# Kernel tuning notes

Hardware: AMD Instinct MI355X
Metric: run time of the kernel (lower is better)

## Reference

```python
import jax, jax.numpy as jnp
import numpy as np

DIM = 1024
NUM_EXPERTS = 8
HIDDEN = 4096
CAP_FACTOR = 2.0
B, S = 4, 2048


def setup_inputs() -> dict:
    key = jax.random.key(0)
    ks = jax.random.split(key, 6)
    scale_r = 1.0 / np.sqrt(DIM)
    scale_1 = 1.0 / np.sqrt(DIM)
    scale_2 = 1.0 / np.sqrt(HIDDEN)
    return {
        "x": jax.random.normal(ks[0], (B, S, DIM), dtype=jnp.float32),
        # router: nn.Linear(dim, num_experts, bias=False) -> weight [E, D]
        "router_w": jax.random.uniform(ks[1], (NUM_EXPERTS, DIM), jnp.float32, -scale_r, scale_r),
        # stacked expert MLP params
        "w1": jax.random.uniform(ks[2], (NUM_EXPERTS, DIM, HIDDEN), jnp.float32, -scale_1, scale_1),
        "b1": jax.random.uniform(ks[3], (NUM_EXPERTS, HIDDEN), jnp.float32, -scale_1, scale_1),
        "w2": jax.random.uniform(ks[4], (NUM_EXPERTS, HIDDEN, DIM), jnp.float32, -scale_2, scale_2),
        "b2": jax.random.uniform(ks[5], (NUM_EXPERTS, DIM), jnp.float32, -scale_2, scale_2),
    }


def reference(x, router_w, w1, b1, w2, b2):
    # x: [B, S, D]
    Bz, Sz, Dz = x.shape
    E = router_w.shape[0]
    capacity = max(1, int(Sz * CAP_FACTOR / E) + 1)

    # router softmax over experts: [B, S, E]
    scores = jax.nn.softmax(jnp.einsum("bsd,ed->bse", x, router_w), axis=-1)

    # expert-choice: each expert picks top-C tokens. [B, E, S] -> [B, E, C]
    scores_t = jnp.swapaxes(scores, 1, 2)
    gate_vals, sel_idx = jax.lax.top_k(scores_t, capacity)

    # gather selected tokens: [B, E, C, D]
    b_idx = jnp.arange(Bz)[:, None, None]
    tokens = x[b_idx, sel_idx]

    # batched expert MLP (GELU exact, matching nn.GELU default)
    h = jnp.einsum("becd,edh->bech", tokens, w1) + b1[None, :, None, :]
    h = jax.nn.gelu(h, approximate=False)
    y = jnp.einsum("bech,ehd->becd", h, w2) + b2[None, :, None, :]

    # gate and scatter-add combine back to [B, S, D]
    gated = y * gate_vals[..., None]
    out = jnp.zeros_like(x).at[b_idx, sel_idx].add(gated)
    return out
```

## Files before the change

kernel.cpp:

```cpp
#include <hip/hip_runtime.h>
#include <cstdint>

#define DIMD  1024
#define NEXP  8
#define HIDN  4096
#define BATCH 4
#define SEQ   2048
#define CAPC  513
#define RPEX  2176
#define TPEX  17
#define MTOT  (NEXP * RPEX)
#define MTILES (MTOT / 128)

typedef __bf16 bf16x8 __attribute__((ext_vector_type(8)));
typedef float  f32x4  __attribute__((ext_vector_type(4)));

__device__ __forceinline__ unsigned short f2bf(float f) {
    unsigned u = __float_as_uint(f);
    unsigned r = (u + 0x7FFFu + ((u >> 16) & 1u)) >> 16;
    return (unsigned short)r;
}

__device__ __forceinline__ void gl16(const unsigned short* g, unsigned short* l) {
    __builtin_amdgcn_global_load_lds(
        (const __attribute__((address_space(1))) void*)g,
        (__attribute__((address_space(3))) void*)l, 16, 0, 0);
}

__device__ __forceinline__ void swz_grp(int GY, int& bx, int& by) {
    int xcd = blockIdx.x & 7, pos = blockIdx.x >> 3;
    int tps = TPEX * GY;
    int sc = pos / tps, rem = pos - sc * tps;
    int bxl = rem / GY, byIn = rem - bxl * GY;
    bx = xcd * TPEX + bxl;
    by = sc * GY + byIn;
}

__global__ __launch_bounds__(64)
void router_kernel(const float* __restrict__ x, const float* __restrict__ rw,
                   float* __restrict__ scores) {
    int token = blockIdx.x;
    int lane  = threadIdx.x;
    const float4* xr = reinterpret_cast<const float4*>(x + (size_t)token * DIMD);
    float4 xv[4];
#pragma unroll
    for (int j = 0; j < 4; ++j) xv[j] = xr[lane * 4 + j];
    float acc[NEXP];
#pragma unroll
    for (int e = 0; e < NEXP; ++e) {
        const float4* wr = reinterpret_cast<const float4*>(rw + (size_t)e * DIMD);
        float a = 0.f;
#pragma unroll
        for (int j = 0; j < 4; ++j) {
            float4 wv = wr[lane * 4 + j];
            a += xv[j].x * wv.x; a += xv[j].y * wv.y;
            a += xv[j].z * wv.z; a += xv[j].w * wv.w;
        }
#pragma unroll
        for (int off = 32; off > 0; off >>= 1) a += __shfl_xor(a, off);
        acc[e] = a;
    }
    float m = acc[0];
#pragma unroll
    for (int e = 1; e < NEXP; ++e) m = fmaxf(m, acc[e]);
    float s = 0.f;
#pragma unroll
    for (int e = 0; e < NEXP; ++e) { acc[e] = expf(acc[e] - m); s += acc[e]; }
    float inv = 1.f / s;
    if (lane == 0) {
        int b = token >> 11;
        int t = token & (SEQ - 1);
#pragma unroll
        for (int e = 0; e < NEXP; ++e)
            scores[((size_t)(b * NEXP + e)) * SEQ + t] = acc[e] * inv;
    }
}

__global__ __launch_bounds__(256)
void topk_kernel(const float* __restrict__ scores, int* __restrict__ sel,
                 float* __restrict__ gate, int* __restrict__ cnt,
                 int* __restrict__ invmap) {
    int be    = blockIdx.x >> 3;
    int chunk = blockIdx.x & 7;
    const float* sc = scores + (size_t)be * SEQ;
    __shared__ float s_sc[SEQ];
    int t = threadIdx.x;
#pragma unroll
    for (int q = 0; q < 8; ++q) s_sc[t + q * 256] = sc[t + q * 256];
    __syncthreads();
    int i = chunk * 256 + t;
    float v = s_sc[i];
    int r = 0;
#pragma unroll 8
    for (int j = 0; j < SEQ; ++j) {
        float u = s_sc[j];
        r += (u > v) || (u == v && j < i);
    }
    if (r < CAPC) {
        sel [(size_t)be * CAPC + r] = i;
        gate[(size_t)be * CAPC + r] = v;
        int b = be >> 3, e = be & 7;
        int tok = b * SEQ + i;
        int p = atomicAdd(cnt + tok, 1);
        invmap[(size_t)tok * 8 + p] = e * RPEX + b * CAPC + r;
    }
}

__global__ __launch_bounds__(256)
void gather_kernel(const float* __restrict__ x, const int* __restrict__ sel,
                   unsigned short* __restrict__ dhi) {
    int gr = blockIdx.x;
    int e  = gr / RPEX;
    int rl = gr - e * RPEX;
    int t  = threadIdx.x;
    size_t dbase = (size_t)gr * DIMD + t * 4;
    if (rl < BATCH * CAPC) {
        int b = rl / CAPC, c = rl - b * CAPC;
        int tok = sel[(size_t)(b * NEXP + e) * CAPC + c];
        float4 v = *reinterpret_cast<const float4*>(x + ((size_t)(b * SEQ + tok)) * DIMD + t * 4);
        ushort4 h;
        h.x = f2bf(v.x); h.y = f2bf(v.y); h.z = f2bf(v.z); h.w = f2bf(v.w);
        *reinterpret_cast<ushort4*>(dhi + dbase) = h;
    } else {
        ushort4 z = {0, 0, 0, 0};
        *reinterpret_cast<ushort4*>(dhi + dbase) = z;
    }
}

__global__ __launch_bounds__(256)
void convT_kernel(const float* __restrict__ src, unsigned short* __restrict__ dhi,
                  int Nsrc, size_t srcEStride, int k0, int n0, int kLen, int nLen) {
    int e = blockIdx.z;
    src += (size_t)e * srcEStride;
    dhi += (size_t)e * kLen * nLen;
    int kb = blockIdx.x * 64, nb = blockIdx.y * 64;
    __shared__ float T[64][65];
    int t = threadIdx.x;
    for (int i = t; i < 1024; i += 256) {
        int r = i >> 4, c4 = (i & 15) * 4;
        float4 v = *reinterpret_cast<const float4*>(
            src + (size_t)(k0 + kb + r) * Nsrc + n0 + nb + c4);
        T[r][c4 + 0] = v.x; T[r][c4 + 1] = v.y; T[r][c4 + 2] = v.z; T[r][c4 + 3] = v.w;
    }
    __syncthreads();
    for (int i = t; i < 1024; i += 256) {
        int n = i >> 4, kc = (i & 15) * 4;
        ushort4 h;
        h.x = f2bf(T[kc + 0][n]); h.y = f2bf(T[kc + 1][n]);
        h.z = f2bf(T[kc + 2][n]); h.w = f2bf(T[kc + 3][n]);
        *reinterpret_cast<ushort4*>(dhi + (size_t)(nb + n) * kLen + kb + kc) = h;
    }
}


#define GEMM_PRE(Abase, Bbase, Kc)                                              \
    int t = threadIdx.x;                                                        \
    int l = t & 63, wid = t >> 6;                                               \
    int wr = wid >> 1, wc = wid & 1;                                            \
    int grp = l >> 4, li = l & 15;                                              \
    int fsw  = (grp ^ ((li >> 1) & 3)) * 8;                                     \
    int gsrc = ((l & 3) ^ ((l >> 3) & 3)) * 8;                                  \
    int ra0 = (wid * 2) * 16 + (l >> 2);                                        \
    int ra1 = ra0 + 16;                                                         \
    __shared__ __align__(16) unsigned short As[3][4096];                        \
    __shared__ __align__(16) unsigned short Bs[3][4096];                        \
    int regA = wid * 1024;                                                      \
    const unsigned short* gA0 = (Abase) + (size_t)(bx * 128 + ra0) * (Kc) + gsrc; \
    const unsigned short* gA1 = (Abase) + (size_t)(bx * 128 + ra1) * (Kc) + gsrc; \
    const unsigned short* gB0 = (Bbase) + (size_t)(bn + ra0) * (Kc) + gsrc;     \
    const unsigned short* gB1 = (Bbase) + (size_t)(bn + ra1) * (Kc) + gsrc;     \
    f32x4 acc[4][4];                                                            \
    _Pragma("unroll")                                                           \
    for (int m = 0; m < 4; ++m)                                                 \
        _Pragma("unroll")                                                       \
        for (int n = 0; n < 4; ++n) { f32x4 z = {0.f,0.f,0.f,0.f}; acc[m][n] = z; }

#define STAGE(buf, kt) do {                                                     \
    gl16(gA0 + (kt), &As[buf][regA]);                                           \
    gl16(gA1 + (kt), &As[buf][regA + 512]);                                     \
    gl16(gB0 + (kt), &Bs[buf][regA]);                                           \
    gl16(gB1 + (kt), &Bs[buf][regA + 512]); } while (0)

#define GEMM_LOOP(Kc) do {                                                      \
    const int NT = (Kc) / 32;                                                   \
    STAGE(0, 0);                                                                \
    STAGE(1, 32);                                                               \
    int cb = 0;                                                                 \
    for (int tt = 0; tt < NT; ++tt) {                                           \
        if (tt == NT - 1) asm volatile("s_waitcnt vmcnt(0)" ::: "memory");      \
        else              asm volatile("s_waitcnt vmcnt(4)" ::: "memory");      \
        __builtin_amdgcn_s_barrier();                                           \
        int sb = cb + 2; if (sb >= 3) sb -= 3;                                  \
        if (tt + 2 < NT) STAGE(sb, (tt + 2) * 32);                              \
        bf16x8 ah[4], bh[4];                                                    \
        const unsigned short* aB = &As[cb][wr * 2048 + li * 32 + fsw];          \
        const unsigned short* bB = &Bs[cb][wc * 2048 + li * 32 + fsw];          \
        ah[0] = *(const bf16x8*)(aB);        ah[1] = *(const bf16x8*)(aB + 512); \
        ah[2] = *(const bf16x8*)(aB + 1024); ah[3] = *(const bf16x8*)(aB + 1536); \
        bh[0] = *(const bf16x8*)(bB);        bh[1] = *(const bf16x8*)(bB + 512); \
        bh[2] = *(const bf16x8*)(bB + 1024); bh[3] = *(const bf16x8*)(bB + 1536); \
        __builtin_amdgcn_s_setprio(1);                                          \
        _Pragma("unroll")                                                       \
        for (int m = 0; m < 4; ++m)                                             \
            _Pragma("unroll")                                                   \
            for (int n = 0; n < 4; ++n)                                         \
                acc[m][n] = __builtin_amdgcn_mfma_f32_16x16x32_bf16(            \
                    ah[m], bh[n], acc[m][n], 0, 0, 0);                          \
        __builtin_amdgcn_s_setprio(0);                                          \
        ++cb; if (cb == 3) cb = 0;                                              \
    } } while (0)

__global__ __launch_bounds__(256)
void gemm1_mfma(const unsigned short* __restrict__ Ahi,
                const unsigned short* __restrict__ Whi,
                const float* __restrict__ bias, unsigned short* __restrict__ Hhi,
                size_t wstride, int nbias0, int ldh, int GY) {
    const int K = DIMD;
    int bx, by; swz_grp(GY, bx, by);
    int bn = by * 128;
    int e = bx / TPEX;
    const unsigned short* Bh = Whi + (size_t)e * wstride;

    GEMM_PRE(Ahi, Bh, K)
    GEMM_LOOP(K);

    int hr0 = bx * 128 + wr * 64;
    int cb2 = bn + wc * 64;
    const float cc0 = 0.044715f;
    const float cc1 = -2.302118131f;
#pragma unroll
    for (int m = 0; m < 4; ++m)
#pragma unroll
        for (int q = 0; q < 4; ++q) {
            int row = hr0 + m * 16 + grp * 4 + q;
#pragma unroll
            for (int n = 0; n < 4; ++n) {
                int col = cb2 + n * 16 + li;
                float v = acc[m][n][q] + bias[(size_t)e * HIDN + nbias0 + col];
                float p = __builtin_fmaf(cc0 * v, v * v, v);
                float g = v * __builtin_amdgcn_rcpf(1.0f + exp2f(cc1 * p));
                Hhi[(size_t)row * ldh + col] = f2bf(g);
            }
        }
}

__global__ __launch_bounds__(256)
void gemm2_mfma(const unsigned short* __restrict__ Ahi,
                const unsigned short* __restrict__ Whi,
                const float* __restrict__ bias, const float* __restrict__ gate,
                float* __restrict__ Y, size_t wstride, int K, int GY) {
    int bx, by; swz_grp(GY, bx, by);
    int bn = by * 128;
    int e = bx / TPEX;
    int rbase_e = (bx - e * TPEX) * 128;
    const unsigned short* Bh = Whi + (size_t)e * wstride;

    GEMM_PRE(Ahi, Bh, K)
    GEMM_LOOP(K);

    int cb2 = bn + wc * 64;
#pragma unroll
    for (int m = 0; m < 4; ++m)
#pragma unroll
        for (int q = 0; q < 4; ++q) {
            int off = wr * 64 + m * 16 + grp * 4 + q;
            int rloc = rbase_e + off;
            if (rloc < BATCH * CAPC) {
                int b = rloc / CAPC, c = rloc - b * CAPC;
                float g = gate[(size_t)(b * NEXP + e) * CAPC + c];
                size_t grow = (size_t)bx * 128 + off;
#pragma unroll
                for (int n = 0; n < 4; ++n) {
                    int col = cb2 + n * 16 + li;
                    float v = acc[m][n][q];
                    size_t yo = grow * DIMD + col;
                    if (bias) Y[yo] = g * (v + bias[(size_t)e * DIMD + col]);
                    else      Y[yo] = Y[yo] + g * v;
                }
            }
        }
}

__global__ __launch_bounds__(64)
void combine_kernel(const float* __restrict__ Y, const int* __restrict__ cnt,
                    const int* __restrict__ invmap, float* __restrict__ out) {
    int tok = blockIdx.x;
    int lane = threadIdx.x;
    int n = cnt[tok];
    f32x4 acc[4];
#pragma unroll
    for (int q = 0; q < 4; ++q) { f32x4 z = {0.f, 0.f, 0.f, 0.f}; acc[q] = z; }
#pragma unroll
    for (int j = 0; j < 8; ++j) {
        if (j < n) {
            int row = invmap[(size_t)tok * 8 + j];
            const f32x4* yr = reinterpret_cast<const f32x4*>(Y + (size_t)row * DIMD);
#pragma unroll
            for (int q = 0; q < 4; ++q) acc[q] += yr[q * 64 + lane];
        }
    }
    f32x4* op = reinterpret_cast<f32x4*>(out + (size_t)tok * DIMD);
#pragma unroll
    for (int q = 0; q < 4; ++q) op[q * 64 + lane] = acc[q];
}

extern "C" void kernel_launch(void* const* d_in, const int* in_sizes, int n_in,
                              void* d_out, int out_size, void* d_ws, size_t ws_size,
                              hipStream_t stream) {
    (void)in_sizes; (void)n_in; (void)out_size;
    const float* x  = (const float*)d_in[0];
    const float* rw = (const float*)d_in[1];
    const float* w1 = (const float*)d_in[2];
    const float* b1 = (const float*)d_in[3];
    const float* w2 = (const float*)d_in[4];
    const float* b2 = (const float*)d_in[5];
    float* out = (float*)d_out;

    char* ws = (char*)d_ws;
    size_t off = 0;
    auto alloc = [&](size_t bytes) -> char* {
        char* p = ws + off;
        off = (off + bytes + 255) & ~(size_t)255;
        return p;
    };

    float* scores = (float*)alloc((size_t)BATCH * NEXP * SEQ * 4);
    int*   sel    = (int*)  alloc((size_t)BATCH * NEXP * CAPC * 4);
    float* gate   = (float*)alloc((size_t)BATCH * NEXP * CAPC * 4);
    int*   cnt    = (int*)  alloc((size_t)BATCH * SEQ * 4);
    int*   invmap = (int*)  alloc((size_t)BATCH * SEQ * 8 * 4);
    float* Y      = (float*)alloc((size_t)MTOT * DIMD * 4);
    size_t common = off;

    const size_t A1B = (size_t)MTOT * DIMD * 2;
    int C = 8;
    for (int c = 1; c <= 8; c <<= 1) {
        size_t wc = (size_t)NEXP * (HIDN / c) * DIMD * 2;
        size_t hc = (size_t)MTOT * (HIDN / c) * 2;
        size_t need = common + A1B + 2 * wc + hc + (8u << 20);
        if (need <= ws_size) { C = c; break; }
    }
    const int HN = HIDN / C;
    const int nY1 = HN / 128;
    const int GY1 = (nY1 < 8) ? nY1 : 8;

    unsigned short* A1h = (unsigned short*)alloc(A1B);
    size_t WCB = (size_t)NEXP * HN * DIMD * 2;
    size_t HCB = (size_t)MTOT * HN * 2;
    unsigned short* W1h = (unsigned short*)alloc(WCB);
    unsigned short* W2h = (unsigned short*)alloc(WCB);
    unsigned short* Hh  = (unsigned short*)alloc(HCB);

    hipMemsetAsync(cnt, 0, (size_t)BATCH * SEQ * 4, stream);
    router_kernel<<<BATCH * SEQ, 64, 0, stream>>>(x, rw, scores);
    topk_kernel<<<BATCH * NEXP * 8, 256, 0, stream>>>(scores, sel, gate, cnt, invmap);
    gather_kernel<<<MTOT, 256, 0, stream>>>(x, sel, A1h);

    for (int c = 0; c < C; ++c) {
        convT_kernel<<<dim3(DIMD / 64, HN / 64, NEXP), 256, 0, stream>>>(
            w1, W1h, HIDN, (size_t)DIMD * HIDN, 0, c * HN, DIMD, HN);
        gemm1_mfma<<<MTILES * nY1, 256, 0, stream>>>(
            A1h, W1h, b1, Hh, (size_t)HN * DIMD, c * HN, HN, GY1);
        convT_kernel<<<dim3(HN / 64, DIMD / 64, NEXP), 256, 0, stream>>>(
            w2, W2h, DIMD, (size_t)HIDN * DIMD, c * HN, 0, HN, DIMD);
        gemm2_mfma<<<MTILES * (DIMD / 128), 256, 0, stream>>>(
            Hh, W2h, (c == 0) ? b2 : nullptr, gate, Y,
            (size_t)DIMD * HN, HN, 4);
    }
    combine_kernel<<<BATCH * SEQ, 64, 0, stream>>>(Y, cnt, invmap, out);
}
```

Before: 619.6 us.

## Widen GEMM tiles to 128x256 and split-K gemm2 into two partial outputs

Both expert GEMMs now use 128x256 output tiles, with each wave computing a 4x8 grid of MFMA fragments and a larger B buffer in shared memory, so each A tile is reused across more columns. gemm2 splits K in two, writing partial sums to separate Y0/Y1 buffers that the combine kernel adds together, which keeps the grid large despite the wider tiles. gemm1 loads its bias values into registers once before the epilogue. The cost is higher register and LDS use per block, which may lower occupancy, plus an extra fp32 Y buffer and more combine traffic.

```diff
diff --git a/kernel.cpp b/kernel.cpp
--- a/kernel.cpp
+++ b/kernel.cpp
@@ -25,15 +25,6 @@
     __builtin_amdgcn_global_load_lds(
         (const __attribute__((address_space(1))) void*)g,
         (__attribute__((address_space(3))) void*)l, 16, 0, 0);
-}
-
-__device__ __forceinline__ void swz_grp(int GY, int& bx, int& by) {
-    int xcd = blockIdx.x & 7, pos = blockIdx.x >> 3;
-    int tps = TPEX * GY;
-    int sc = pos / tps, rem = pos - sc * tps;
-    int bxl = rem / GY, byIn = rem - bxl * GY;
-    bx = xcd * TPEX + bxl;
-    by = sc * GY + byIn;
 }
 
 __global__ __launch_bounds__(64)
@@ -153,79 +144,88 @@
 }
 
 
-#define GEMM_PRE(Abase, Bbase, Kc)                                              \
+#define GEMM_PRE(Abase, LDA, Bbase, LDB)                                        \
     int t = threadIdx.x;                                                        \
     int l = t & 63, wid = t >> 6;                                               \
     int wr = wid >> 1, wc = wid & 1;                                            \
     int grp = l >> 4, li = l & 15;                                              \
     int fsw  = (grp ^ ((li >> 1) & 3)) * 8;                                     \
     int gsrc = ((l & 3) ^ ((l >> 3) & 3)) * 8;                                  \
-    int ra0 = (wid * 2) * 16 + (l >> 2);                                        \
-    int ra1 = ra0 + 16;                                                         \
-    __shared__ __align__(16) unsigned short As[3][4096];                        \
-    __shared__ __align__(16) unsigned short Bs[3][4096];                        \
-    int regA = wid * 1024;                                                      \
-    const unsigned short* gA0 = (Abase) + (size_t)(bx * 128 + ra0) * (Kc) + gsrc; \
-    const unsigned short* gA1 = (Abase) + (size_t)(bx * 128 + ra1) * (Kc) + gsrc; \
-    const unsigned short* gB0 = (Bbase) + (size_t)(bn + ra0) * (Kc) + gsrc;     \
-    const unsigned short* gB1 = (Bbase) + (size_t)(bn + ra1) * (Kc) + gsrc;     \
-    f32x4 acc[4][4];                                                            \
+    __shared__ __align__(16) unsigned short As[3][4096];         \
+    __shared__ __align__(16) unsigned short Bs[3][8192];         \
+    int dst = wid * 512;                                                        \
+    const unsigned short* gA0 = (Abase) + (size_t)(bx * 128 + wid * 16 + (l >> 2)) * (LDA) + gsrc; \
+    const unsigned short* gA1 = gA0 + (size_t)64 * (LDA);                       \
+    const unsigned short* gB0 = (Bbase) + (size_t)(bn + wid * 16 + (l >> 2)) * (LDB) + gsrc; \
+    const unsigned short* gB1 = gB0 + (size_t)64  * (LDB);                      \
+    const unsigned short* gB2 = gB0 + (size_t)128 * (LDB);                      \
+    const unsigned short* gB3 = gB0 + (size_t)192 * (LDB);                      \
+    f32x4 acc[4][8];                                                            \
     _Pragma("unroll")                                                           \
     for (int m = 0; m < 4; ++m)                                                 \
         _Pragma("unroll")                                                       \
-        for (int n = 0; n < 4; ++n) { f32x4 z = {0.f,0.f,0.f,0.f}; acc[m][n] = z; }
+        for (int n = 0; n < 8; ++n) { f32x4 z = {0.f,0.f,0.f,0.f}; acc[m][n] = z; }
 
 #define STAGE(buf, kt) do {                                                     \
-    gl16(gA0 + (kt), &As[buf][regA]);                                           \
-    gl16(gA1 + (kt), &As[buf][regA + 512]);                                     \
-    gl16(gB0 + (kt), &Bs[buf][regA]);                                           \
-    gl16(gB1 + (kt), &Bs[buf][regA + 512]); } while (0)
-
-#define GEMM_LOOP(Kc) do {                                                      \
-    const int NT = (Kc) / 32;                                                   \
+    gl16(gA0 + (kt), &As[buf][dst]);                                            \
+    gl16(gA1 + (kt), &As[buf][2048 + dst]);                                     \
+    gl16(gB0 + (kt), &Bs[buf][dst]);                                            \
+    gl16(gB1 + (kt), &Bs[buf][2048 + dst]);                                     \
+    gl16(gB2 + (kt), &Bs[buf][4096 + dst]);                                     \
+    gl16(gB3 + (kt), &Bs[buf][6144 + dst]); } while (0)
+
+#define GEMM_LOOP(NT) do {                                                      \
     STAGE(0, 0);                                                                \
     STAGE(1, 32);                                                               \
     int cb = 0;                                                                 \
-    for (int tt = 0; tt < NT; ++tt) {                                           \
-        if (tt == NT - 1) asm volatile("s_waitcnt vmcnt(0)" ::: "memory");      \
-        else              asm volatile("s_waitcnt vmcnt(4)" ::: "memory");      \
+    for (int tt = 0; tt < (NT); ++tt) {                                         \
+        if (tt == (NT) - 1) asm volatile("s_waitcnt vmcnt(0)" ::: "memory");    \
+        else                asm volatile("s_waitcnt vmcnt(6)" ::: "memory");    \
         __builtin_amdgcn_s_barrier();                                           \
         int sb = cb + 2; if (sb >= 3) sb -= 3;                                  \
-        if (tt + 2 < NT) STAGE(sb, (tt + 2) * 32);                              \
-        bf16x8 ah[4], bh[4];                                                    \
+        if (tt + 2 < (NT)) STAGE(sb, (tt + 2) * 32);                            \
+        bf16x8 af[4], bfv[8];                                                   \
         const unsigned short* aB = &As[cb][wr * 2048 + li * 32 + fsw];          \
-        const unsigned short* bB = &Bs[cb][wc * 2048 + li * 32 + fsw];          \
-        ah[0] = *(const bf16x8*)(aB);        ah[1] = *(const bf16x8*)(aB + 512); \
-        ah[2] = *(const bf16x8*)(aB + 1024); ah[3] = *(const bf16x8*)(aB + 1536); \
-        bh[0] = *(const bf16x8*)(bB);        bh[1] = *(const bf16x8*)(bB + 512); \
-        bh[2] = *(const bf16x8*)(bB + 1024); bh[3] = *(const bf16x8*)(bB + 1536); \
+        const unsigned short* bB = &Bs[cb][wc * 4096 + li * 32 + fsw];          \
+        _Pragma("unroll")                                                       \
+        for (int m = 0; m < 4; ++m) af[m]  = *(const bf16x8*)(aB + m * 512);    \
+        _Pragma("unroll")                                                       \
+        for (int n = 0; n < 8; ++n) bfv[n] = *(const bf16x8*)(bB + n * 512);    \
         __builtin_amdgcn_s_setprio(1);                                          \
         _Pragma("unroll")                                                       \
         for (int m = 0; m < 4; ++m)                                             \
             _Pragma("unroll")                                                   \
-            for (int n = 0; n < 4; ++n)                                         \
+            for (int n = 0; n < 8; ++n)                                         \
                 acc[m][n] = __builtin_amdgcn_mfma_f32_16x16x32_bf16(            \
-                    ah[m], bh[n], acc[m][n], 0, 0, 0);                          \
+                    af[m], bfv[n], acc[m][n], 0, 0, 0);                         \
         __builtin_amdgcn_s_setprio(0);                                          \
         ++cb; if (cb == 3) cb = 0;                                              \
     } } while (0)
 
 __global__ __launch_bounds__(256)
-void gemm1_mfma(const unsigned short* __restrict__ Ahi,
-                const unsigned short* __restrict__ Whi,
+void gemm1_mfma(const unsigned short* __restrict__ A,
+                const unsigned short* __restrict__ W,
                 const float* __restrict__ bias, unsigned short* __restrict__ Hhi,
                 size_t wstride, int nbias0, int ldh, int GY) {
     const int K = DIMD;
-    int bx, by; swz_grp(GY, bx, by);
-    int bn = by * 128;
+    int xcd = blockIdx.x & 7, pos = blockIdx.x >> 3;
+    int tps = TPEX * GY;
+    int sc = pos / tps, rem = pos - sc * tps;
+    int bxl = rem / GY, byIn = rem - bxl * GY;
+    int bx = xcd * TPEX + bxl;
+    int bn = (sc * GY + byIn) * 256;
     int e = bx / TPEX;
-    const unsigned short* Bh = Whi + (size_t)e * wstride;
-
-    GEMM_PRE(Ahi, Bh, K)
-    GEMM_LOOP(K);
+    const unsigned short* Bb = W + (size_t)e * wstride;
+
+    GEMM_PRE(A, K, Bb, K)
+    GEMM_LOOP(K / 32);
 
     int hr0 = bx * 128 + wr * 64;
-    int cb2 = bn + wc * 64;
+    int cb2 = bn + wc * 128;
+    float bv[8];
+#pragma unroll
+    for (int n = 0; n < 8; ++n)
+        bv[n] = bias[(size_t)e * HIDN + nbias0 + cb2 + n * 16 + li];
     const float cc0 = 0.044715f;
     const float cc1 = -2.302118131f;
 #pragma unroll
@@ -234,9 +234,9 @@
         for (int q = 0; q < 4; ++q) {
             int row = hr0 + m * 16 + grp * 4 + q;
 #pragma unroll
-            for (int n = 0; n < 4; ++n) {
+            for (int n = 0; n < 8; ++n) {
                 int col = cb2 + n * 16 + li;
-                float v = acc[m][n][q] + bias[(size_t)e * HIDN + nbias0 + col];
+                float v = acc[m][n][q] + bv[n];
                 float p = __builtin_fmaf(cc0 * v, v * v, v);
                 float g = v * __builtin_amdgcn_rcpf(1.0f + exp2f(cc1 * p));
                 Hhi[(size_t)row * ldh + col] = f2bf(g);
@@ -245,20 +245,28 @@
 }
 
 __global__ __launch_bounds__(256)
-void gemm2_mfma(const unsigned short* __restrict__ Ahi,
-                const unsigned short* __restrict__ Whi,
-                const float* __restrict__ bias, const float* __restrict__ gate,
-                float* __restrict__ Y, size_t wstride, int K, int GY) {
-    int bx, by; swz_grp(GY, bx, by);
-    int bn = by * 128;
+void gemm2_mfma(const unsigned short* __restrict__ Hh,
+                const unsigned short* __restrict__ W2,
+                const float* __restrict__ bias, int init,
+                const float* __restrict__ gate,
+                float* __restrict__ Y0, float* __restrict__ Y1,
+                size_t wstride, int lda, int Kb) {
+    int xcd = blockIdx.x & 7, pos = blockIdx.x >> 3;
+    int ks = pos / (TPEX * 4);
+    int rem = pos - ks * (TPEX * 4);
+    int bxl = rem >> 2, by = rem & 3;
+    int bx = xcd * TPEX + bxl;
+    int bn = by * 256;
     int e = bx / TPEX;
     int rbase_e = (bx - e * TPEX) * 128;
-    const unsigned short* Bh = Whi + (size_t)e * wstride;
-
-    GEMM_PRE(Ahi, Bh, K)
-    GEMM_LOOP(K);
-
-    int cb2 = bn + wc * 64;
+    const unsigned short* Ab = Hh + (size_t)ks * Kb;
+    const unsigned short* Bb = W2 + (size_t)e * wstride + (size_t)ks * Kb;
+
+    GEMM_PRE(Ab, lda, Bb, lda)
+    GEMM_LOOP(Kb / 32);
+
+    float* Yp = ks ? Y1 : Y0;
+    int cb2 = bn + wc * 128;
 #pragma unroll
     for (int m = 0; m < 4; ++m)
 #pragma unroll
@@ -270,20 +278,22 @@
                 float g = gate[(size_t)(b * NEXP + e) * CAPC + c];
                 size_t grow = (size_t)bx * 128 + off;
 #pragma unroll
-                for (int n = 0; n < 4; ++n) {
+                for (int n = 0; n < 8; ++n) {
                     int col = cb2 + n * 16 + li;
                     float v = acc[m][n][q];
+                    if (ks == 0 && bias) v += bias[(size_t)e * DIMD + col];
                     size_t yo = grow * DIMD + col;
-                    if (bias) Y[yo] = g * (v + bias[(size_t)e * DIMD + col]);
-                    else      Y[yo] = Y[yo] + g * v;
+                    if (init) Yp[yo] = g * v;
+                    else      Yp[yo] = Yp[yo] + g * v;
                 }
             }
         }
 }
 
 __global__ __launch_bounds__(64)
-void combine_kernel(const float* __restrict__ Y, const int* __restrict__ cnt,
-                    const int* __restrict__ invmap, float* __restrict__ out) {
+void combine_kernel(const float* __restrict__ Y0, const float* __restrict__ Y1,
+                    const int* __restrict__ cnt, const int* __restrict__ invmap,
+                    float* __restrict__ out) {
     int tok = blockIdx.x;
     int lane = threadIdx.x;
     int n = cnt[tok];
@@ -294,9 +304,10 @@
     for (int j = 0; j < 8; ++j) {
         if (j < n) {
             int row = invmap[(size_t)tok * 8 + j];
-            const f32x4* yr = reinterpret_cast<const f32x4*>(Y + (size_t)row * DIMD);
-#pragma unroll
-            for (int q = 0; q < 4; ++q) acc[q] += yr[q * 64 + lane];
+            const f32x4* y0 = reinterpret_cast<const f32x4*>(Y0 + (size_t)row * DIMD);
+            const f32x4* y1 = reinterpret_cast<const f32x4*>(Y1 + (size_t)row * DIMD);
+#pragma unroll
+            for (int q = 0; q < 4; ++q) acc[q] += y0[q * 64 + lane] + y1[q * 64 + lane];
         }
     }
     f32x4* op = reinterpret_cast<f32x4*>(out + (size_t)tok * DIMD);
@@ -329,7 +340,8 @@
     float* gate   = (float*)alloc((size_t)BATCH * NEXP * CAPC * 4);
     int*   cnt    = (int*)  alloc((size_t)BATCH * SEQ * 4);
     int*   invmap = (int*)  alloc((size_t)BATCH * SEQ * 8 * 4);
-    float* Y      = (float*)alloc((size_t)MTOT * DIMD * 4);
+    float* Y0     = (float*)alloc((size_t)MTOT * DIMD * 4);
+    float* Y1     = (float*)alloc((size_t)MTOT * DIMD * 4);
     size_t common = off;
 
     const size_t A1B = (size_t)MTOT * DIMD * 2;
@@ -341,8 +353,8 @@
         if (need <= ws_size) { C = c; break; }
     }
     const int HN = HIDN / C;
-    const int nY1 = HN / 128;
-    const int GY1 = (nY1 < 8) ? nY1 : 8;
+    const int nY1 = HN / 256;
+    const int GY1 = (nY1 < 4) ? nY1 : 4;
 
     unsigned short* A1h = (unsigned short*)alloc(A1B);
     size_t WCB = (size_t)NEXP * HN * DIMD * 2;
@@ -363,9 +375,9 @@
             A1h, W1h, b1, Hh, (size_t)HN * DIMD, c * HN, HN, GY1);
         convT_kernel<<<dim3(HN / 64, DIMD / 64, NEXP), 256, 0, stream>>>(
             w2, W2h, DIMD, (size_t)HIDN * DIMD, c * HN, 0, HN, DIMD);
-        gemm2_mfma<<<MTILES * (DIMD / 128), 256, 0, stream>>>(
-            Hh, W2h, (c == 0) ? b2 : nullptr, gate, Y,
-            (size_t)DIMD * HN, HN, 4);
-    }
-    combine_kernel<<<BATCH * SEQ, 64, 0, stream>>>(Y, cnt, invmap, out);
-}
+        gemm2_mfma<<<MTILES * 4 * 2, 256, 0, stream>>>(
+            Hh, W2h, (c == 0) ? b2 : nullptr, (c == 0) ? 1 : 0, gate, Y0, Y1,
+            (size_t)DIMD * HN, HN, HN / 2);
+    }
+    combine_kernel<<<BATCH * SEQ, 64, 0, stream>>>(Y0, Y1, cnt, invmap, out);
+}
```

Result: slower. 957.1 us (+54.5%).

## Split-K the second expert GEMM into two partial outputs summed in combine

Applied to the files above, without the earlier changes.

The down-projection GEMM now splits its K dimension in two, launching twice as many workgroups. Each half writes to its own fp32 buffer (Y0/Y1), and the combine kernel sums both. Block indexing is remapped so each XCD gets a contiguous set of M tiles, improving L2 locality. The goal is to fill the GPU better when the grid of 136x8 tiles underutilizes the CUs, at the cost of an extra 70MB fp32 buffer write/read and doubled combine reads.

```diff
diff --git a/kernel.cpp b/kernel.cpp
--- a/kernel.cpp
+++ b/kernel.cpp
@@ -153,7 +153,7 @@
 }
 
 
-#define GEMM_PRE(Abase, Bbase, Kc)                                              \
+#define GEMM_PRE(Abase, LDA, Bbase, LDB)                                        \
     int t = threadIdx.x;                                                        \
     int l = t & 63, wid = t >> 6;                                               \
     int wr = wid >> 1, wc = wid & 1;                                            \
@@ -165,10 +165,10 @@
     __shared__ __align__(16) unsigned short As[3][4096];                        \
     __shared__ __align__(16) unsigned short Bs[3][4096];                        \
     int regA = wid * 1024;                                                      \
-    const unsigned short* gA0 = (Abase) + (size_t)(bx * 128 + ra0) * (Kc) + gsrc; \
-    const unsigned short* gA1 = (Abase) + (size_t)(bx * 128 + ra1) * (Kc) + gsrc; \
-    const unsigned short* gB0 = (Bbase) + (size_t)(bn + ra0) * (Kc) + gsrc;     \
-    const unsigned short* gB1 = (Bbase) + (size_t)(bn + ra1) * (Kc) + gsrc;     \
+    const unsigned short* gA0 = (Abase) + (size_t)(bx * 128 + ra0) * (LDA) + gsrc; \
+    const unsigned short* gA1 = (Abase) + (size_t)(bx * 128 + ra1) * (LDA) + gsrc; \
+    const unsigned short* gB0 = (Bbase) + (size_t)(bn + ra0) * (LDB) + gsrc;    \
+    const unsigned short* gB1 = (Bbase) + (size_t)(bn + ra1) * (LDB) + gsrc;    \
     f32x4 acc[4][4];                                                            \
     _Pragma("unroll")                                                           \
     for (int m = 0; m < 4; ++m)                                                 \
@@ -181,17 +181,16 @@
     gl16(gB0 + (kt), &Bs[buf][regA]);                                           \
     gl16(gB1 + (kt), &Bs[buf][regA + 512]); } while (0)
 
-#define GEMM_LOOP(Kc) do {                                                      \
-    const int NT = (Kc) / 32;                                                   \
+#define GEMM_LOOP(NT) do {                                                      \
     STAGE(0, 0);                                                                \
     STAGE(1, 32);                                                               \
     int cb = 0;                                                                 \
-    for (int tt = 0; tt < NT; ++tt) {                                           \
-        if (tt == NT - 1) asm volatile("s_waitcnt vmcnt(0)" ::: "memory");      \
-        else              asm volatile("s_waitcnt vmcnt(4)" ::: "memory");      \
+    for (int tt = 0; tt < (NT); ++tt) {                                         \
+        if (tt == (NT) - 1) asm volatile("s_waitcnt vmcnt(0)" ::: "memory");    \
+        else                asm volatile("s_waitcnt vmcnt(4)" ::: "memory");    \
         __builtin_amdgcn_s_barrier();                                           \
         int sb = cb + 2; if (sb >= 3) sb -= 3;                                  \
-        if (tt + 2 < NT) STAGE(sb, (tt + 2) * 32);                              \
+        if (tt + 2 < (NT)) STAGE(sb, (tt + 2) * 32);                            \
         bf16x8 ah[4], bh[4];                                                    \
         const unsigned short* aB = &As[cb][wr * 2048 + li * 32 + fsw];          \
         const unsigned short* bB = &Bs[cb][wc * 2048 + li * 32 + fsw];          \
@@ -221,8 +220,8 @@
     int e = bx / TPEX;
     const unsigned short* Bh = Whi + (size_t)e * wstride;
 
-    GEMM_PRE(Ahi, Bh, K)
-    GEMM_LOOP(K);
+    GEMM_PRE(Ahi, K, Bh, K)
+    GEMM_LOOP(K / 32);
 
     int hr0 = bx * 128 + wr * 64;
     int cb2 = bn + wc * 64;
@@ -245,19 +244,27 @@
 }
 
 __global__ __launch_bounds__(256)
-void gemm2_mfma(const unsigned short* __restrict__ Ahi,
-                const unsigned short* __restrict__ Whi,
-                const float* __restrict__ bias, const float* __restrict__ gate,
-                float* __restrict__ Y, size_t wstride, int K, int GY) {
-    int bx, by; swz_grp(GY, bx, by);
+void gemm2_mfma(const unsigned short* __restrict__ Hh,
+                const unsigned short* __restrict__ W2,
+                const float* __restrict__ bias, int init,
+                const float* __restrict__ gate,
+                float* __restrict__ Y0, float* __restrict__ Y1,
+                size_t wstride, int lda, int Kb) {
+    int xcd = blockIdx.x & 7, pos = blockIdx.x >> 3;
+    int ks = pos / (TPEX * 8);
+    int rem = pos - ks * (TPEX * 8);
+    int bxl = rem >> 3, by = rem & 7;
+    int bx = xcd * TPEX + bxl;
     int bn = by * 128;
     int e = bx / TPEX;
     int rbase_e = (bx - e * TPEX) * 128;
-    const unsigned short* Bh = Whi + (size_t)e * wstride;
-
-    GEMM_PRE(Ahi, Bh, K)
-    GEMM_LOOP(K);
-
+    const unsigned short* Ab = Hh + (size_t)ks * Kb;
+    const unsigned short* Bb = W2 + (size_t)e * wstride + (size_t)ks * Kb;
+
+    GEMM_PRE(Ab, lda, Bb, lda)
+    GEMM_LOOP(Kb / 32);
+
+    float* Yp = ks ? Y1 : Y0;
     int cb2 = bn + wc * 64;
 #pragma unroll
     for (int m = 0; m < 4; ++m)
@@ -273,17 +280,19 @@
                 for (int n = 0; n < 4; ++n) {
                     int col = cb2 + n * 16 + li;
                     float v = acc[m][n][q];
+                    if (ks == 0 && bias) v += bias[(size_t)e * DIMD + col];
                     size_t yo = grow * DIMD + col;
-                    if (bias) Y[yo] = g * (v + bias[(size_t)e * DIMD + col]);
-                    else      Y[yo] = Y[yo] + g * v;
+                    if (init) Yp[yo] = g * v;
+                    else      Yp[yo] = Yp[yo] + g * v;
                 }
             }
         }
 }
 
 __global__ __launch_bounds__(64)
-void combine_kernel(const float* __restrict__ Y, const int* __restrict__ cnt,
-                    const int* __restrict__ invmap, float* __restrict__ out) {
+void combine_kernel(const float* __restrict__ Y0, const float* __restrict__ Y1,
+                    const int* __restrict__ cnt, const int* __restrict__ invmap,
+                    float* __restrict__ out) {
     int tok = blockIdx.x;
     int lane = threadIdx.x;
     int n = cnt[tok];
@@ -294,9 +303,10 @@
     for (int j = 0; j < 8; ++j) {
         if (j < n) {
             int row = invmap[(size_t)tok * 8 + j];
-            const f32x4* yr = reinterpret_cast<const f32x4*>(Y + (size_t)row * DIMD);
-#pragma unroll
-            for (int q = 0; q < 4; ++q) acc[q] += yr[q * 64 + lane];
+            const f32x4* y0 = reinterpret_cast<const f32x4*>(Y0 + (size_t)row * DIMD);
+            const f32x4* y1 = reinterpret_cast<const f32x4*>(Y1 + (size_t)row * DIMD);
+#pragma unroll
+            for (int q = 0; q < 4; ++q) acc[q] += y0[q * 64 + lane] + y1[q * 64 + lane];
         }
     }
     f32x4* op = reinterpret_cast<f32x4*>(out + (size_t)tok * DIMD);
@@ -329,7 +339,8 @@
     float* gate   = (float*)alloc((size_t)BATCH * NEXP * CAPC * 4);
     int*   cnt    = (int*)  alloc((size_t)BATCH * SEQ * 4);
     int*   invmap = (int*)  alloc((size_t)BATCH * SEQ * 8 * 4);
-    float* Y      = (float*)alloc((size_t)MTOT * DIMD * 4);
+    float* Y0     = (float*)alloc((size_t)MTOT * DIMD * 4);
+    float* Y1     = (float*)alloc((size_t)MTOT * DIMD * 4);
     size_t common = off;
 
     const size_t A1B = (size_t)MTOT * DIMD * 2;
@@ -363,9 +374,9 @@
             A1h, W1h, b1, Hh, (size_t)HN * DIMD, c * HN, HN, GY1);
         convT_kernel<<<dim3(HN / 64, DIMD / 64, NEXP), 256, 0, stream>>>(
             w2, W2h, DIMD, (size_t)HIDN * DIMD, c * HN, 0, HN, DIMD);
-        gemm2_mfma<<<MTILES * (DIMD / 128), 256, 0, stream>>>(
-            Hh, W2h, (c == 0) ? b2 : nullptr, gate, Y,
-            (size_t)DIMD * HN, HN, 4);
-    }
-    combine_kernel<<<BATCH * SEQ, 64, 0, stream>>>(Y, cnt, invmap, out);
-}
+        gemm2_mfma<<<MTILES * 8 * 2, 256, 0, stream>>>(
+            Hh, W2h, (c == 0) ? b2 : nullptr, (c == 0) ? 1 : 0, gate, Y0, Y1,
+            (size_t)DIMD * HN, HN, HN / 2);
+    }
+    combine_kernel<<<BATCH * SEQ, 64, 0, stream>>>(Y0, Y1, cnt, invmap, out);
+}
```

Result: no change. 620.5 us, median of 2 (+0.2%).

## Fold weight transpose-convert blocks into topk and GEMM launches for overlap

Applied to the files above, without the earlier changes.

Removes the standalone convT launches and instead appends extra blocks to the topk, gemm1 and gemm2 grids that transpose and convert the next weight chunk. The W1 conversion overlaps with topk, W2 with gemm1, and the next W1 chunk with gemm2. This saves launch gaps and lets memory-bound conversion run alongside compute. It relies on the chunked workspace being double-buffered correctly, and the extra blocks share the GEMM shared-memory footprint.

```diff
diff --git a/kernel.cpp b/kernel.cpp
--- a/kernel.cpp
+++ b/kernel.cpp
@@ -76,14 +76,48 @@
     }
 }
 
+__device__ __forceinline__ void convT_body(const float* __restrict__ src,
+        unsigned short* __restrict__ dhi, int Nsrc, size_t srcEStride,
+        int k0, int n0, int kLen, int nLen, int cid, float (*T)[65]) {
+    int nx = kLen >> 6, ny = nLen >> 6;
+    int e = cid / (nx * ny);
+    int r2 = cid - e * nx * ny;
+    int kb = (r2 % nx) * 64, nb = (r2 / nx) * 64;
+    src += (size_t)e * srcEStride;
+    dhi += (size_t)e * (size_t)kLen * nLen;
+    int t = threadIdx.x;
+    for (int i = t; i < 1024; i += 256) {
+        int r = i >> 4, c4 = (i & 15) * 4;
+        float4 v = *reinterpret_cast<const float4*>(
+            src + (size_t)(k0 + kb + r) * Nsrc + n0 + nb + c4);
+        T[r][c4 + 0] = v.x; T[r][c4 + 1] = v.y; T[r][c4 + 2] = v.z; T[r][c4 + 3] = v.w;
+    }
+    __syncthreads();
+    for (int i = t; i < 1024; i += 256) {
+        int n = i >> 4, kc = (i & 15) * 4;
+        ushort4 h;
+        h.x = f2bf(T[kc + 0][n]); h.y = f2bf(T[kc + 1][n]);
+        h.z = f2bf(T[kc + 2][n]); h.w = f2bf(T[kc + 3][n]);
+        *reinterpret_cast<ushort4*>(dhi + (size_t)(nb + n) * kLen + kb + kc) = h;
+    }
+}
+
 __global__ __launch_bounds__(256)
-void topk_kernel(const float* __restrict__ scores, int* __restrict__ sel,
-                 float* __restrict__ gate, int* __restrict__ cnt,
-                 int* __restrict__ invmap) {
+void topk_conv1(const float* __restrict__ scores, int* __restrict__ sel,
+                float* __restrict__ gate, int* __restrict__ cnt,
+                int* __restrict__ invmap,
+                const float* __restrict__ csrc, unsigned short* __restrict__ cdst,
+                int cNsrc, size_t cEStride, int ck0, int cn0, int ckLen, int cnLen) {
+    __shared__ __align__(16) float T[64][65];
+    if ((int)blockIdx.x >= 256) {
+        convT_body(csrc, cdst, cNsrc, cEStride, ck0, cn0, ckLen, cnLen,
+                   blockIdx.x - 256, T);
+        return;
+    }
+    float* s_sc = &T[0][0];
     int be    = blockIdx.x >> 3;
     int chunk = blockIdx.x & 7;
     const float* sc = scores + (size_t)be * SEQ;
-    __shared__ float s_sc[SEQ];
     int t = threadIdx.x;
 #pragma unroll
     for (int q = 0; q < 8; ++q) s_sc[t + q * 256] = sc[t + q * 256];
@@ -127,33 +161,8 @@
     }
 }
 
-__global__ __launch_bounds__(256)
-void convT_kernel(const float* __restrict__ src, unsigned short* __restrict__ dhi,
-                  int Nsrc, size_t srcEStride, int k0, int n0, int kLen, int nLen) {
-    int e = blockIdx.z;
-    src += (size_t)e * srcEStride;
-    dhi += (size_t)e * kLen * nLen;
-    int kb = blockIdx.x * 64, nb = blockIdx.y * 64;
-    __shared__ float T[64][65];
-    int t = threadIdx.x;
-    for (int i = t; i < 1024; i += 256) {
-        int r = i >> 4, c4 = (i & 15) * 4;
-        float4 v = *reinterpret_cast<const float4*>(
-            src + (size_t)(k0 + kb + r) * Nsrc + n0 + nb + c4);
-        T[r][c4 + 0] = v.x; T[r][c4 + 1] = v.y; T[r][c4 + 2] = v.z; T[r][c4 + 3] = v.w;
-    }
-    __syncthreads();
-    for (int i = t; i < 1024; i += 256) {
-        int n = i >> 4, kc = (i & 15) * 4;
-        ushort4 h;
-        h.x = f2bf(T[kc + 0][n]); h.y = f2bf(T[kc + 1][n]);
-        h.z = f2bf(T[kc + 2][n]); h.w = f2bf(T[kc + 3][n]);
-        *reinterpret_cast<ushort4*>(dhi + (size_t)(nb + n) * kLen + kb + kc) = h;
-    }
-}
-
-
-#define GEMM_PRE(Abase, Bbase, Kc)                                              \
+
+#define GEMM_PRE(Abase, LDA, Bbase, LDB)                                        \
     int t = threadIdx.x;                                                        \
     int l = t & 63, wid = t >> 6;                                               \
     int wr = wid >> 1, wc = wid & 1;                                            \
@@ -162,13 +171,11 @@
     int gsrc = ((l & 3) ^ ((l >> 3) & 3)) * 8;                                  \
     int ra0 = (wid * 2) * 16 + (l >> 2);                                        \
     int ra1 = ra0 + 16;                                                         \
-    __shared__ __align__(16) unsigned short As[3][4096];                        \
-    __shared__ __align__(16) unsigned short Bs[3][4096];                        \
     int regA = wid * 1024;                                                      \
-    const unsigned short* gA0 = (Abase) + (size_t)(bx * 128 + ra0) * (Kc) + gsrc; \
-    const unsigned short* gA1 = (Abase) + (size_t)(bx * 128 + ra1) * (Kc) + gsrc; \
-    const unsigned short* gB0 = (Bbase) + (size_t)(bn + ra0) * (Kc) + gsrc;     \
-    const unsigned short* gB1 = (Bbase) + (size_t)(bn + ra1) * (Kc) + gsrc;     \
+    const unsigned short* gA0 = (Abase) + (size_t)(bx * 128 + ra0) * (LDA) + gsrc; \
+    const unsigned short* gA1 = (Abase) + (size_t)(bx * 128 + ra1) * (LDA) + gsrc; \
+    const unsigned short* gB0 = (Bbase) + (size_t)(bn + ra0) * (LDB) + gsrc;    \
+    const unsigned short* gB1 = (Bbase) + (size_t)(bn + ra1) * (LDB) + gsrc;    \
     f32x4 acc[4][4];                                                            \
     _Pragma("unroll")                                                           \
     for (int m = 0; m < 4; ++m)                                                 \
@@ -181,17 +188,16 @@
     gl16(gB0 + (kt), &Bs[buf][regA]);                                           \
     gl16(gB1 + (kt), &Bs[buf][regA + 512]); } while (0)
 
-#define GEMM_LOOP(Kc) do {                                                      \
-    const int NT = (Kc) / 32;                                                   \
+#define GEMM_LOOP(NT) do {                                                      \
     STAGE(0, 0);                                                                \
     STAGE(1, 32);                                                               \
     int cb = 0;                                                                 \
-    for (int tt = 0; tt < NT; ++tt) {                                           \
-        if (tt == NT - 1) asm volatile("s_waitcnt vmcnt(0)" ::: "memory");      \
-        else              asm volatile("s_waitcnt vmcnt(4)" ::: "memory");      \
+    for (int tt = 0; tt < (NT); ++tt) {                                         \
+        if (tt == (NT) - 1) asm volatile("s_waitcnt vmcnt(0)" ::: "memory");    \
+        else                asm volatile("s_waitcnt vmcnt(4)" ::: "memory");    \
         __builtin_amdgcn_s_barrier();                                           \
         int sb = cb + 2; if (sb >= 3) sb -= 3;                                  \
-        if (tt + 2 < NT) STAGE(sb, (tt + 2) * 32);                              \
+        if (tt + 2 < (NT)) STAGE(sb, (tt + 2) * 32);                            \
         bf16x8 ah[4], bh[4];                                                    \
         const unsigned short* aB = &As[cb][wr * 2048 + li * 32 + fsw];          \
         const unsigned short* bB = &Bs[cb][wc * 2048 + li * 32 + fsw];          \
@@ -214,15 +220,24 @@
 void gemm1_mfma(const unsigned short* __restrict__ Ahi,
                 const unsigned short* __restrict__ Whi,
                 const float* __restrict__ bias, unsigned short* __restrict__ Hhi,
-                size_t wstride, int nbias0, int ldh, int GY) {
+                size_t wstride, int nbias0, int ldh, int GY, int nGemm,
+                const float* __restrict__ csrc, unsigned short* __restrict__ cdst,
+                int cNsrc, size_t cEStride, int ck0, int cn0, int ckLen, int cnLen) {
+    __shared__ __align__(16) unsigned short As[3][4096];
+    __shared__ __align__(16) unsigned short Bs[3][4096];
+    if ((int)blockIdx.x >= nGemm) {
+        convT_body(csrc, cdst, cNsrc, cEStride, ck0, cn0, ckLen, cnLen,
+                   blockIdx.x - nGemm, reinterpret_cast<float(*)[65]>(&As[0][0]));
+        return;
+    }
     const int K = DIMD;
     int bx, by; swz_grp(GY, bx, by);
     int bn = by * 128;
     int e = bx / TPEX;
     const unsigned short* Bh = Whi + (size_t)e * wstride;
 
-    GEMM_PRE(Ahi, Bh, K)
-    GEMM_LOOP(K);
+    GEMM_PRE(Ahi, K, Bh, K)
+    GEMM_LOOP(K / 32);
 
     int hr0 = bx * 128 + wr * 64;
     int cb2 = bn + wc * 64;
@@ -245,18 +260,27 @@
 }
 
 __global__ __launch_bounds__(256)
-void gemm2_mfma(const unsigned short* __restrict__ Ahi,
-                const unsigned short* __restrict__ Whi,
+void gemm2_mfma(const unsigned short* __restrict__ Hh,
+                const unsigned short* __restrict__ W2,
                 const float* __restrict__ bias, const float* __restrict__ gate,
-                float* __restrict__ Y, size_t wstride, int K, int GY) {
+                float* __restrict__ Y, size_t wstride, int K, int GY, int nGemm,
+                const float* __restrict__ csrc, unsigned short* __restrict__ cdst,
+                int cNsrc, size_t cEStride, int ck0, int cn0, int ckLen, int cnLen) {
+    __shared__ __align__(16) unsigned short As[3][4096];
+    __shared__ __align__(16) unsigned short Bs[3][4096];
+    if ((int)blockIdx.x >= nGemm) {
+        convT_body(csrc, cdst, cNsrc, cEStride, ck0, cn0, ckLen, cnLen,
+                   blockIdx.x - nGemm, reinterpret_cast<float(*)[65]>(&As[0][0]));
+        return;
+    }
     int bx, by; swz_grp(GY, bx, by);
     int bn = by * 128;
     int e = bx / TPEX;
     int rbase_e = (bx - e * TPEX) * 128;
-    const unsigned short* Bh = Whi + (size_t)e * wstride;
-
-    GEMM_PRE(Ahi, Bh, K)
-    GEMM_LOOP(K);
+    const unsigned short* Bb = W2 + (size_t)e * wstride;
+
+    GEMM_PRE(Hh, K, Bb, K)
+    GEMM_LOOP(K / 32);
 
     int cb2 = bn + wc * 64;
 #pragma unroll
@@ -351,21 +375,27 @@
     unsigned short* W2h = (unsigned short*)alloc(WCB);
     unsigned short* Hh  = (unsigned short*)alloc(HCB);
 
+    const int nCv1 = (DIMD / 64) * (HN / 64) * NEXP;
+    const int nCv2 = (HN / 64) * (DIMD / 64) * NEXP;
+
     hipMemsetAsync(cnt, 0, (size_t)BATCH * SEQ * 4, stream);
     router_kernel<<<BATCH * SEQ, 64, 0, stream>>>(x, rw, scores);
-    topk_kernel<<<BATCH * NEXP * 8, 256, 0, stream>>>(scores, sel, gate, cnt, invmap);
+    topk_conv1<<<256 + nCv1, 256, 0, stream>>>(
+        scores, sel, gate, cnt, invmap,
+        w1, W1h, HIDN, (size_t)DIMD * HIDN, 0, 0, DIMD, HN);
     gather_kernel<<<MTOT, 256, 0, stream>>>(x, sel, A1h);
 
     for (int c = 0; c < C; ++c) {
-        convT_kernel<<<dim3(DIMD / 64, HN / 64, NEXP), 256, 0, stream>>>(
-            w1, W1h, HIDN, (size_t)DIMD * HIDN, 0, c * HN, DIMD, HN);
-        gemm1_mfma<<<MTILES * nY1, 256, 0, stream>>>(
-            A1h, W1h, b1, Hh, (size_t)HN * DIMD, c * HN, HN, GY1);
-        convT_kernel<<<dim3(HN / 64, DIMD / 64, NEXP), 256, 0, stream>>>(
+        int G1 = MTILES * nY1;
+        gemm1_mfma<<<G1 + nCv2, 256, 0, stream>>>(
+            A1h, W1h, b1, Hh, (size_t)HN * DIMD, c * HN, HN, GY1, G1,
             w2, W2h, DIMD, (size_t)HIDN * DIMD, c * HN, 0, HN, DIMD);
-        gemm2_mfma<<<MTILES * (DIMD / 128), 256, 0, stream>>>(
+        int G2 = MTILES * (DIMD / 128);
+        int more = (c + 1 < C) ? nCv1 : 0;
+        gemm2_mfma<<<G2 + more, 256, 0, stream>>>(
             Hh, W2h, (c == 0) ? b2 : nullptr, gate, Y,
-            (size_t)DIMD * HN, HN, 4);
+            (size_t)DIMD * HN, HN, 4, G2,
+            w1, W1h, HIDN, (size_t)DIMD * HIDN, 0, (c + 1) * HN, DIMD, HN);
     }
     combine_kernel<<<BATCH * SEQ, 64, 0, stream>>>(Y, cnt, invmap, out);
 }
```

After: 569.7 us (median of 2 runs). -8.1%, faster.
